# Optimization experiments

Hardware: AMD Instinct MI355X
Metric: run time of the kernel (lower is better)

## Reference

```python
import jax, jax.numpy as jnp
import numpy as np

B, C, L, T = 8, 512, 2048, 64

def setup_inputs() -> dict:
    key = jax.random.key(0)
    k1, k2, k3 = jax.random.split(key, 3)
    x = jax.random.normal(k1, (B, C, 1, L), dtype=jnp.float32)
    W1 = jax.random.normal(k2, (T, C), dtype=jnp.float32) * (1.0 / np.sqrt(C))
    W2 = jax.random.normal(k3, (T, C), dtype=jnp.float32) * (1.0 / np.sqrt(C))
    gamma = jnp.ones((1, 1), dtype=jnp.float32)
    ranges = 0  # unused by forward
    return {"x": x, "W1": W1, "W2": W2, "gamma": gamma, "ranges": ranges}

def reference(x, W1, W2, gamma, ranges):
    temp = x[:, :, 0, :]                                  # (B, C, L)
    q = jnp.einsum('tc,bcl->btl', W1, temp)               # conv1x1 -> (B, T, L)
    k = jnp.einsum('tc,bcl->btl', W2, temp)               # conv1x1 -> (B, T, L)
    scores = jnp.einsum('btl,btm->blm', q, k)             # Q^T K -> (B, L, L)
    attn = jax.nn.softmax(scores, axis=2)                 # softmax over last dim
    # temp @ attn^T: out[:, :, j] = sum_i attn[j, i] * temp[:, :, i]
    out = jnp.einsum('bci,bji->bcj', temp, attn)          # (B, C, L)
    out = temp + gamma[0, 0] * out                        # gamma scale + residual
    return out[:, :, None, :]                             # (B, C, 1, L)
```

## Files before the change

### kernel.cpp

```cpp
#include <hip/hip_runtime.h>
#include <cstddef>

#define BB 8
#define CC 512
#define LL 2048
#define TT 64

typedef short short8 __attribute__((ext_vector_type(8)));
typedef float floatx4 __attribute__((ext_vector_type(4)));
typedef unsigned short b16u;
typedef unsigned int u32;

static __device__ __forceinline__ unsigned f2bfu(float f) {
    unsigned u = __float_as_uint(f);
    u += 0x7fffu + ((u >> 16) & 1u);
    return u >> 16;
}
static __device__ __forceinline__ float bfu2f(unsigned h) {
    return __uint_as_float(h << 16);
}

#define MFMA16(a, b, c) __builtin_amdgcn_mfma_f32_16x16x32_bf16((a), (b), (c), 0, 0, 0)

__global__ __launch_bounds__(256) void wcvt_kernel(
    const float* __restrict__ W1, const float* __restrict__ W2,
    b16u* __restrict__ W1h, b16u* __restrict__ W1l,
    b16u* __restrict__ W2h, b16u* __restrict__ W2l)
{
    int flat = blockIdx.x * 256 + threadIdx.x;
    float4 v1 = *(const float4*)(W1 + (size_t)flat * 4);
    float4 v2 = *(const float4*)(W2 + (size_t)flat * 4);
    const float* e1 = (const float*)&v1;
    const float* e2 = (const float*)&v2;
    unsigned h1[4], l1[4], h2[4], l2[4];
#pragma unroll
    for (int k = 0; k < 4; ++k) {
        h1[k] = f2bfu(e1[k]); l1[k] = f2bfu(e1[k] - bfu2f(h1[k]));
        h2[k] = f2bfu(e2[k]); l2[k] = f2bfu(e2[k] - bfu2f(h2[k]));
    }
    uint2 a, b, c, d;
    a.x = h1[0] | (h1[1] << 16); a.y = h1[2] | (h1[3] << 16);
    b.x = l1[0] | (l1[1] << 16); b.y = l1[2] | (l1[3] << 16);
    c.x = h2[0] | (h2[1] << 16); c.y = h2[2] | (h2[3] << 16);
    d.x = l2[0] | (l2[1] << 16); d.y = l2[2] | (l2[3] << 16);
    *(uint2*)(W1h + (size_t)flat * 4) = a;
    *(uint2*)(W1l + (size_t)flat * 4) = b;
    *(uint2*)(W2h + (size_t)flat * 4) = c;
    *(uint2*)(W2l + (size_t)flat * 4) = d;
}

__global__ __launch_bounds__(256) void qkcvt_kernel(
    const float* __restrict__ x,
    const b16u* __restrict__ W1h, const b16u* __restrict__ W1l,
    const b16u* __restrict__ W2h, const b16u* __restrict__ W2l,
    b16u* __restrict__ Qt, b16u* __restrict__ Kt)
{
    __shared__ b16u Sxh[64 * 72];
    __shared__ b16u Sxl[64 * 72];
    __shared__ b16u S1h[64 * 72];
    __shared__ b16u S1l[64 * 72];
    __shared__ b16u S2h[64 * 72];
    __shared__ b16u S2l[64 * 72];
    const int b  = blockIdx.y;
    const int l0 = blockIdx.x * 64;
    const int tid = threadIdx.x;
    const int lane = tid & 63;
    const int w = tid >> 6;
    const int n16 = lane & 15;
    const int qd = lane >> 4;
    const float* xb = x + (size_t)b * CC * LL;

    const int cx = tid >> 2;
    const int sx = tid & 3;

    float4 xreg[4];
#pragma unroll
    for (int p = 0; p < 4; ++p)
        xreg[p] = *(const float4*)(xb + (size_t)cx * LL + l0 + (sx * 4 + p) * 4);

    floatx4 aq[4], ak[4];
#pragma unroll
    for (int nt = 0; nt < 4; ++nt) {
        aq[nt] = (floatx4){0.f, 0.f, 0.f, 0.f};
        ak[nt] = (floatx4){0.f, 0.f, 0.f, 0.f};
    }

    for (int c0 = 0; c0 < 512; c0 += 64) {
        __syncthreads();
#pragma unroll
        for (int p = 0; p < 4; ++p) {
            const float* e = (const float*)&xreg[p];
            int lbase = (sx * 4 + p) * 4;
#pragma unroll
            for (int k = 0; k < 4; ++k) {
                unsigned h = f2bfu(e[k]);
                unsigned lo = f2bfu(e[k] - bfu2f(h));
                Sxh[(lbase + k) * 72 + cx] = (b16u)h;
                Sxl[(lbase + k) * 72 + cx] = (b16u)lo;
            }
        }
#pragma unroll
        for (int p = 0; p < 2; ++p) {
            int flat = tid + p * 256;
            int t = flat >> 3, s8 = flat & 7;
            size_t off = (size_t)t * 512 + c0 + s8 * 8;
            *(uint4*)&S1h[t * 72 + s8 * 8] = *(const uint4*)(W1h + off);
            *(uint4*)&S1l[t * 72 + s8 * 8] = *(const uint4*)(W1l + off);
            *(uint4*)&S2h[t * 72 + s8 * 8] = *(const uint4*)(W2h + off);
            *(uint4*)&S2l[t * 72 + s8 * 8] = *(const uint4*)(W2l + off);
        }
        __syncthreads();
        if (c0 < 448) {
#pragma unroll
            for (int p = 0; p < 4; ++p)
                xreg[p] = *(const float4*)(xb + (size_t)(c0 + 64 + cx) * LL +
                                           l0 + (sx * 4 + p) * 4);
        }
#pragma unroll
        for (int kc = 0; kc < 2; ++kc) {
            const int ao = (w * 16 + n16) * 72 + kc * 32 + qd * 8;
            short8 a1h = *(const short8*)&S1h[ao];
            short8 a1l = *(const short8*)&S1l[ao];
            short8 a2h = *(const short8*)&S2h[ao];
            short8 a2l = *(const short8*)&S2l[ao];
#pragma unroll
            for (int nt = 0; nt < 4; ++nt) {
                const int bo = (nt * 16 + n16) * 72 + kc * 32 + qd * 8;
                short8 bh = *(const short8*)&Sxh[bo];
                short8 bl = *(const short8*)&Sxl[bo];
                aq[nt] = MFMA16(a1h, bh, aq[nt]);
                aq[nt] = MFMA16(a1h, bl, aq[nt]);
                aq[nt] = MFMA16(a1l, bh, aq[nt]);
                ak[nt] = MFMA16(a2h, bh, ak[nt]);
                ak[nt] = MFMA16(a2h, bl, ak[nt]);
                ak[nt] = MFMA16(a2l, bh, ak[nt]);
            }
        }
    }
#pragma unroll
    for (int nt = 0; nt < 4; ++nt) {
        int l = l0 + nt * 16 + n16;
        uint2 pq, pk;
        pq.x = f2bfu(aq[nt][0]) | (f2bfu(aq[nt][1]) << 16);
        pq.y = f2bfu(aq[nt][2]) | (f2bfu(aq[nt][3]) << 16);
        pk.x = f2bfu(ak[nt][0]) | (f2bfu(ak[nt][1]) << 16);
        pk.y = f2bfu(ak[nt][2]) | (f2bfu(ak[nt][3]) << 16);
        *(uint2*)(Qt + ((size_t)(b * 2048) + l) * 64 + w * 16 + qd * 4) = pq;
        *(uint2*)(Kt + ((size_t)(b * 2048) + l) * 64 + w * 16 + qd * 4) = pk;
    }
}

__global__ __launch_bounds__(256) void xcvt_kernel(
    const float* __restrict__ x, b16u* __restrict__ XT)
{
    int flat = blockIdx.x * 256 + threadIdx.x;
    int i4 = flat & 15;
    int t  = (flat >> 4) & 31;
    int c  = (flat >> 9) & 511;
    int b  = flat >> 18;
    float4 v = *(const float4*)(x + ((size_t)(b * 512 + c)) * 2048 + t * 64 + i4 * 4);
    uint2 wv;
    wv.x = f2bfu(v.x) | (f2bfu(v.y) << 16);
    wv.y = f2bfu(v.z) | (f2bfu(v.w) << 16);
    *(uint2*)(XT + (((size_t)(b * 32) + t) * 512 + c) * 64 + i4 * 4) = wv;
}

__global__ __launch_bounds__(512, 2) void fused_kernel(
    const float* __restrict__ x, const b16u* __restrict__ XT,
    const b16u* __restrict__ Qt, const b16u* __restrict__ Kt,
    const float* __restrict__ gamma, float* __restrict__ out)
{
    __shared__ __align__(16) char smem[139776];
    b16u*  Ps = (b16u*)smem;
    float* Zw = (float*)(smem + 32768);
    float* Zf = (float*)(smem + 139264);

    const int bid = blockIdx.x;
    const int b   = bid & 7;
    const int c0  = ((bid >> 3) & 1) * 256;
    const int j0  = (bid >> 4) * 128;
    const int tid = threadIdx.x;
    const int lane = tid & 63;
    const int w    = tid >> 6;
    const int n16  = lane & 15;
    const int qd   = lane >> 4;
    const int wi   = w & 3;
    const int wh   = w >> 2;

    const b16u* Qb = Qt + ((size_t)(b * LL) + j0 + wh * 64 + n16) * 64 + qd * 8;
    const b16u* Kb = Kt + ((size_t)(b * LL) + wi * 16 + n16) * 64 + qd * 8;
    const b16u* Vb = XT + (size_t)b * (32 * 512 * 64) +
                     ((size_t)(c0 + wi * 64 + n16)) * 64 + qd * 8;

    short8 qf[4][2];
#pragma unroll
    for (int nt2 = 0; nt2 < 4; ++nt2)
#pragma unroll
        for (int kc = 0; kc < 2; ++kc)
            qf[nt2][kc] = *(const short8*)(Qb + nt2 * (16 * 64) + kc * 32);

    floatx4 acc[4][4];
#pragma unroll
    for (int mt = 0; mt < 4; ++mt)
#pragma unroll
        for (int nt = 0; nt < 4; ++nt) acc[mt][nt] = (floatx4){0.f, 0.f, 0.f, 0.f};
    float zacc[4] = {0.f, 0.f, 0.f, 0.f};

#define KLOAD(KR, T)                                                       \
    {                                                                      \
        const b16u* kp = Kb + (size_t)(T) * (64 * 64);                     \
        KR[0] = *(const short8*)(kp);                                      \
        KR[1] = *(const short8*)(kp + 32);                                 \
    }

#define VLOAD(VR, T)                                                       \
    {                                                                      \
        const b16u* vp = Vb + (size_t)(T) * 32768;                         \
        _Pragma("unroll")                                                  \
        for (int mt = 0; mt < 4; ++mt) {                                   \
            VR[mt][0] = *(const short8*)(vp + mt * 1024);                  \
            VR[mt][1] = *(const short8*)(vp + mt * 1024 + 32);             \
        }                                                                  \
    }

#define SSTEP(PSOFF, KR)                                                   \
    {                                                                      \
        _Pragma("unroll")                                                  \
        for (int nt2 = 0; nt2 < 4; ++nt2) {                                \
            floatx4 sacc = (floatx4){0.f, 0.f, 0.f, 0.f};                  \
            sacc = MFMA16(KR[0], qf[nt2][0], sacc);                        \
            sacc = MFMA16(KR[1], qf[nt2][1], sacc);                        \
            float p0 = __expf(sacc[0] - 20.0f);                            \
            float p1 = __expf(sacc[1] - 20.0f);                            \
            float p2 = __expf(sacc[2] - 20.0f);                            \
            float p3 = __expf(sacc[3] - 20.0f);                            \
            zacc[nt2] += (p0 + p1) + (p2 + p3);                            \
            uint2 pk;                                                      \
            pk.x = f2bfu(p0) | (f2bfu(p1) << 16);                          \
            pk.y = f2bfu(p2) | (f2bfu(p3) << 16);                          \
            int jl = wh * 64 + nt2 * 16 + n16;                             \
            int phys = (wi * 2 + (qd >> 1)) ^ (n16 & 7);                   \
            *(uint2*)&Ps[(PSOFF) + jl * 64 + phys * 8 + (qd & 1) * 4] = pk;\
        }                                                                  \
    }

#define PVSTEP(PSOFF, VR)                                                  \
    {                                                                      \
        __builtin_amdgcn_s_setprio(1);                                     \
        _Pragma("unroll")                                                  \
        for (int kc = 0; kc < 2; ++kc) {                                   \
            short8 bfr[4];                                                 \
            _Pragma("unroll")                                              \
            for (int nt = 0; nt < 4; ++nt) {                               \
                int phys = (kc * 4 + qd) ^ (n16 & 7);                      \
                bfr[nt] = *(const short8*)&Ps[(PSOFF) +                    \
                    (wh * 64 + nt * 16 + n16) * 64 + phys * 8];            \
            }                                                              \
            _Pragma("unroll")                                              \
            for (int mt = 0; mt < 4; ++mt)                                 \
                _Pragma("unroll")                                          \
                for (int nt = 0; nt < 4; ++nt)                             \
                    acc[mt][nt] = MFMA16(VR[mt][kc], bfr[nt], acc[mt][nt]);\
        }                                                                  \
        __builtin_amdgcn_s_setprio(0);                                     \
    }

    short8 kA[2], kB[2], kT[2];
    short8 v0[4][2], v1[4][2];

    KLOAD(kT, 0)
    VLOAD(v0, 0)
    SSTEP(0, kT)
    KLOAD(kA, 1)
    __syncthreads();

    for (int tt = 0; tt < 32; tt += 2) {
        VLOAD(v1, tt + 1)
        if (tt + 2 < 32) KLOAD(kB, tt + 2)
        SSTEP(8192, kA)
        PVSTEP(0, v0)
        __syncthreads();
        if (tt + 2 < 32) {
            VLOAD(v0, tt + 2)
            if (tt + 3 < 32) KLOAD(kA, tt + 3)
            SSTEP(0, kB)
        }
        PVSTEP(8192, v1)
        __syncthreads();
    }
#undef KLOAD
#undef VLOAD
#undef SSTEP
#undef PVSTEP

#pragma unroll
    for (int nt2 = 0; nt2 < 4; ++nt2) {
        float z = zacc[nt2];
        z += __shfl_xor(z, 16);
        z += __shfl_xor(z, 32);
        if (qd == 0) Zw[w * 64 + nt2 * 16 + n16] = z;
    }
    __syncthreads();
    if (tid < 128) {
        int hb = (tid >> 6) * 4;
        Zf[tid] = Zw[(hb + 0) * 64 + (tid & 63)] + Zw[(hb + 1) * 64 + (tid & 63)] +
                  Zw[(hb + 2) * 64 + (tid & 63)] + Zw[(hb + 3) * 64 + (tid & 63)];
    }
    __syncthreads();

    const float g = gamma[0];
    float* st = (float*)(smem + w * 17408);
#pragma unroll
    for (int nt = 0; nt < 4; ++nt) {
        float zi = g / Zf[wh * 64 + nt * 16 + n16];
#pragma unroll
        for (int mt = 0; mt < 4; ++mt)
#pragma unroll
            for (int r = 0; r < 4; ++r)
                st[(mt * 16 + qd * 4 + r) * 68 + nt * 16 + n16] = acc[mt][nt][r] * zi;
    }
    __syncthreads();
#pragma unroll
    for (int p = 0; p < 16; ++p) {
        int rl = qd * 16 + p;
        int cg = c0 + wi * 64 + rl;
        size_t go = ((size_t)(b * CC) + cg) * 2048 + j0 + wh * 64 + n16 * 4;
        float4 v = *(const float4*)&st[rl * 68 + n16 * 4];
        float4 xv = *(const float4*)(x + go);
        v.x += xv.x; v.y += xv.y; v.z += xv.z; v.w += xv.w;
        *(float4*)(out + go) = v;
    }
}

extern "C" void kernel_launch(void* const* d_in, const int* in_sizes, int n_in,
                              void* d_out, int out_size, void* d_ws, size_t ws_size,
                              hipStream_t stream)
{
    (void)in_sizes; (void)n_in; (void)out_size; (void)ws_size;
    const float* x     = (const float*)d_in[0];
    const float* W1    = (const float*)d_in[1];
    const float* W2    = (const float*)d_in[2];
    const float* gamma = (const float*)d_in[3];
    float* out = (float*)d_out;

    b16u* Qt  = (b16u*)d_ws;
    b16u* Kt  = Qt  + (size_t)BB * LL * TT;
    b16u* W1h = Kt  + (size_t)BB * LL * TT;
    b16u* W1l = W1h + (size_t)TT * CC;
    b16u* W2h = W1l + (size_t)TT * CC;
    b16u* W2l = W2h + (size_t)TT * CC;
    b16u* XT  = W2l + (size_t)TT * CC;

    wcvt_kernel <<<dim3(32),      256, 0, stream>>>(W1, W2, W1h, W1l, W2h, W2l);
    xcvt_kernel <<<dim3(8192),    256, 0, stream>>>(x, XT);
    qkcvt_kernel<<<dim3(32, BB),  256, 0, stream>>>(x, W1h, W1l, W2h, W2l, Qt, Kt);
    fused_kernel<<<dim3(256),     512, 0, stream>>>(x, XT, Qt, Kt, gamma, out);
}
```

Baseline: 193.2 us.

## Warp-specialize fused attention into score producers and PV consumers

The fused kernel now runs 12 waves per block. Four producer waves compute QK scores, exponentiate them and write bf16 P tiles into a double-buffered LDS region. Eight consumer waves load V and run the PV MFMAs over all 512 channels for a 64-column query tile. This removes the duplicated score and exp work that the old per-channel-half blocks repeated. The trade-off is that each block now streams twice as much V per query column, and producers and consumers must stay balanced across the barriers.

```diff
diff --git a/kernel.cpp b/kernel.cpp
--- a/kernel.cpp
+++ b/kernel.cpp
@@ -165,86 +165,75 @@
     *(uint2*)(XT + (((size_t)(b * 32) + t) * 512 + c) * 64 + i4 * 4) = wv;
 }
 
-__global__ __launch_bounds__(512, 2) void fused_kernel(
+__global__ __launch_bounds__(768, 3) void fused_kernel(
     const float* __restrict__ x, const b16u* __restrict__ XT,
     const b16u* __restrict__ Qt, const b16u* __restrict__ Kt,
     const float* __restrict__ gamma, float* __restrict__ out)
 {
-    __shared__ __align__(16) char smem[139776];
+    __shared__ __align__(16) char smem[140544];
     b16u*  Ps = (b16u*)smem;
-    float* Zw = (float*)(smem + 32768);
-    float* Zf = (float*)(smem + 139264);
+    float* Zw = (float*)(smem + 139264);
+    float* Zf = (float*)(smem + 140288);
 
     const int bid = blockIdx.x;
     const int b   = bid & 7;
-    const int c0  = ((bid >> 3) & 1) * 256;
-    const int j0  = (bid >> 4) * 128;
+    const int j0  = (bid >> 3) * 64;
     const int tid = threadIdx.x;
     const int lane = tid & 63;
     const int w    = tid >> 6;
     const int n16  = lane & 15;
     const int qd   = lane >> 4;
-    const int wi   = w & 3;
-    const int wh   = w >> 2;
-
-    const b16u* Qb = Qt + ((size_t)(b * LL) + j0 + wh * 64 + n16) * 64 + qd * 8;
-    const b16u* Kb = Kt + ((size_t)(b * LL) + wi * 16 + n16) * 64 + qd * 8;
-    const b16u* Vb = XT + (size_t)b * (32 * 512 * 64) +
-                     ((size_t)(c0 + wi * 64 + n16)) * 64 + qd * 8;
+
+    const b16u* Qb = Qt + ((size_t)(b * LL) + j0 + n16) * 64 + qd * 8;
+    const b16u* Kb = Kt + ((size_t)(b * LL) + (w & 3) * 16 + n16) * 64 + qd * 8;
+    const b16u* Vb = XT + (size_t)b * (32 * 32768) +
+                     ((size_t)((w - 4) * 64 + n16)) * 64 + qd * 8;
 
     short8 qf[4][2];
-#pragma unroll
-    for (int nt2 = 0; nt2 < 4; ++nt2)
-#pragma unroll
-        for (int kc = 0; kc < 2; ++kc)
-            qf[nt2][kc] = *(const short8*)(Qb + nt2 * (16 * 64) + kc * 32);
-
+    short8 kA[2], kB[2];
+    float  zacc[4] = {0.f, 0.f, 0.f, 0.f};
     floatx4 acc[4][4];
-#pragma unroll
-    for (int mt = 0; mt < 4; ++mt)
-#pragma unroll
-        for (int nt = 0; nt < 4; ++nt) acc[mt][nt] = (floatx4){0.f, 0.f, 0.f, 0.f};
-    float zacc[4] = {0.f, 0.f, 0.f, 0.f};
+    short8 av[4][2];
 
 #define KLOAD(KR, T)                                                       \
     {                                                                      \
-        const b16u* kp = Kb + (size_t)(T) * (64 * 64);                     \
+        const b16u* kp = Kb + (size_t)(T) * 4096;                          \
         KR[0] = *(const short8*)(kp);                                      \
         KR[1] = *(const short8*)(kp + 32);                                 \
     }
 
-#define VLOAD(VR, T)                                                       \
+#define VLOAD(T)                                                           \
     {                                                                      \
         const b16u* vp = Vb + (size_t)(T) * 32768;                         \
         _Pragma("unroll")                                                  \
         for (int mt = 0; mt < 4; ++mt) {                                   \
-            VR[mt][0] = *(const short8*)(vp + mt * 1024);                  \
-            VR[mt][1] = *(const short8*)(vp + mt * 1024 + 32);             \
+            av[mt][0] = *(const short8*)(vp + mt * 1024);                  \
+            av[mt][1] = *(const short8*)(vp + mt * 1024 + 32);             \
         }                                                                  \
     }
 
 #define SSTEP(PSOFF, KR)                                                   \
     {                                                                      \
         _Pragma("unroll")                                                  \
-        for (int nt2 = 0; nt2 < 4; ++nt2) {                                \
+        for (int nt = 0; nt < 4; ++nt) {                                   \
             floatx4 sacc = (floatx4){0.f, 0.f, 0.f, 0.f};                  \
-            sacc = MFMA16(KR[0], qf[nt2][0], sacc);                        \
-            sacc = MFMA16(KR[1], qf[nt2][1], sacc);                        \
+            sacc = MFMA16(KR[0], qf[nt][0], sacc);                         \
+            sacc = MFMA16(KR[1], qf[nt][1], sacc);                         \
             float p0 = __expf(sacc[0] - 20.0f);                            \
             float p1 = __expf(sacc[1] - 20.0f);                            \
             float p2 = __expf(sacc[2] - 20.0f);                            \
             float p3 = __expf(sacc[3] - 20.0f);                            \
-            zacc[nt2] += (p0 + p1) + (p2 + p3);                            \
+            zacc[nt] += (p0 + p1) + (p2 + p3);                             \
             uint2 pk;                                                      \
             pk.x = f2bfu(p0) | (f2bfu(p1) << 16);                          \
             pk.y = f2bfu(p2) | (f2bfu(p3) << 16);                          \
-            int jl = wh * 64 + nt2 * 16 + n16;                             \
-            int phys = (wi * 2 + (qd >> 1)) ^ (n16 & 7);                   \
+            int jl = nt * 16 + n16;                                        \
+            int phys = ((w & 3) * 2 + (qd >> 1)) ^ (n16 & 7);              \
             *(uint2*)&Ps[(PSOFF) + jl * 64 + phys * 8 + (qd & 1) * 4] = pk;\
         }                                                                  \
     }
 
-#define PVSTEP(PSOFF, VR)                                                  \
+#define PVSTEP(PSOFF)                                                      \
     {                                                                      \
         __builtin_amdgcn_s_setprio(1);                                     \
         _Pragma("unroll")                                                  \
@@ -254,38 +243,54 @@
             for (int nt = 0; nt < 4; ++nt) {                               \
                 int phys = (kc * 4 + qd) ^ (n16 & 7);                      \
                 bfr[nt] = *(const short8*)&Ps[(PSOFF) +                    \
-                    (wh * 64 + nt * 16 + n16) * 64 + phys * 8];            \
+                    (nt * 16 + n16) * 64 + phys * 8];                      \
             }                                                              \
             _Pragma("unroll")                                              \
             for (int mt = 0; mt < 4; ++mt)                                 \
                 _Pragma("unroll")                                          \
                 for (int nt = 0; nt < 4; ++nt)                             \
-                    acc[mt][nt] = MFMA16(VR[mt][kc], bfr[nt], acc[mt][nt]);\
+                    acc[mt][nt] = MFMA16(av[mt][kc], bfr[nt], acc[mt][nt]);\
         }                                                                  \
         __builtin_amdgcn_s_setprio(0);                                     \
     }
 
-    short8 kA[2], kB[2], kT[2];
-    short8 v0[4][2], v1[4][2];
-
-    KLOAD(kT, 0)
-    VLOAD(v0, 0)
-    SSTEP(0, kT)
-    KLOAD(kA, 1)
+    if (w < 4) {
+#pragma unroll
+        for (int nt = 0; nt < 4; ++nt) {
+            qf[nt][0] = *(const short8*)(Qb + nt * 1024);
+            qf[nt][1] = *(const short8*)(Qb + nt * 1024 + 32);
+        }
+        KLOAD(kA, 0)
+        SSTEP(0, kA)
+        KLOAD(kA, 1)
+    } else {
+#pragma unroll
+        for (int mt = 0; mt < 4; ++mt)
+#pragma unroll
+            for (int nt = 0; nt < 4; ++nt)
+                acc[mt][nt] = (floatx4){0.f, 0.f, 0.f, 0.f};
+        VLOAD(0)
+    }
     __syncthreads();
 
     for (int tt = 0; tt < 32; tt += 2) {
-        VLOAD(v1, tt + 1)
-        if (tt + 2 < 32) KLOAD(kB, tt + 2)
-        SSTEP(8192, kA)
-        PVSTEP(0, v0)
+        if (w < 4) {
+            SSTEP(4096, kA)
+            if (tt + 2 < 32) KLOAD(kB, tt + 2)
+        } else {
+            PVSTEP(0)
+            VLOAD(tt + 1)
+        }
         __syncthreads();
-        if (tt + 2 < 32) {
-            VLOAD(v0, tt + 2)
-            if (tt + 3 < 32) KLOAD(kA, tt + 3)
-            SSTEP(0, kB)
-        }
-        PVSTEP(8192, v1)
+        if (w < 4) {
+            if (tt + 2 < 32) {
+                SSTEP(0, kB)
+                if (tt + 3 < 32) KLOAD(kA, tt + 3)
+            }
+        } else {
+            PVSTEP(4096)
+            if (tt + 2 < 32) VLOAD(tt + 2)
+        }
         __syncthreads();
     }
 #undef KLOAD
@@ -293,42 +298,47 @@
 #undef SSTEP
 #undef PVSTEP
 
-#pragma unroll
-    for (int nt2 = 0; nt2 < 4; ++nt2) {
-        float z = zacc[nt2];
-        z += __shfl_xor(z, 16);
-        z += __shfl_xor(z, 32);
-        if (qd == 0) Zw[w * 64 + nt2 * 16 + n16] = z;
+    if (w < 4) {
+#pragma unroll
+        for (int nt = 0; nt < 4; ++nt) {
+            float z = zacc[nt];
+            z += __shfl_xor(z, 16);
+            z += __shfl_xor(z, 32);
+            if (qd == 0) Zw[w * 64 + nt * 16 + n16] = z;
+        }
     }
     __syncthreads();
-    if (tid < 128) {
-        int hb = (tid >> 6) * 4;
-        Zf[tid] = Zw[(hb + 0) * 64 + (tid & 63)] + Zw[(hb + 1) * 64 + (tid & 63)] +
-                  Zw[(hb + 2) * 64 + (tid & 63)] + Zw[(hb + 3) * 64 + (tid & 63)];
-    }
+    if (tid < 64)
+        Zf[tid] = Zw[tid] + Zw[64 + tid] + Zw[128 + tid] + Zw[192 + tid];
     __syncthreads();
 
     const float g = gamma[0];
-    float* st = (float*)(smem + w * 17408);
-#pragma unroll
-    for (int nt = 0; nt < 4; ++nt) {
-        float zi = g / Zf[wh * 64 + nt * 16 + n16];
-#pragma unroll
-        for (int mt = 0; mt < 4; ++mt)
-#pragma unroll
-            for (int r = 0; r < 4; ++r)
-                st[(mt * 16 + qd * 4 + r) * 68 + nt * 16 + n16] = acc[mt][nt][r] * zi;
+    if (w >= 4) {
+        float* st = (float*)(smem + (w - 4) * 17408);
+#pragma unroll
+        for (int nt = 0; nt < 4; ++nt) {
+            float zi = g / Zf[nt * 16 + n16];
+#pragma unroll
+            for (int mt = 0; mt < 4; ++mt)
+#pragma unroll
+                for (int r = 0; r < 4; ++r)
+                    st[(mt * 16 + qd * 4 + r) * 68 + nt * 16 + n16] =
+                        acc[mt][nt][r] * zi;
+        }
     }
     __syncthreads();
-#pragma unroll
-    for (int p = 0; p < 16; ++p) {
-        int rl = qd * 16 + p;
-        int cg = c0 + wi * 64 + rl;
-        size_t go = ((size_t)(b * CC) + cg) * 2048 + j0 + wh * 64 + n16 * 4;
-        float4 v = *(const float4*)&st[rl * 68 + n16 * 4];
-        float4 xv = *(const float4*)(x + go);
-        v.x += xv.x; v.y += xv.y; v.z += xv.z; v.w += xv.w;
-        *(float4*)(out + go) = v;
+    if (w >= 4) {
+        const float* st = (const float*)(smem + (w - 4) * 17408);
+#pragma unroll
+        for (int p = 0; p < 16; ++p) {
+            int rl = qd * 16 + p;
+            int cg = (w - 4) * 64 + rl;
+            size_t go = ((size_t)(b * CC) + cg) * 2048 + j0 + n16 * 4;
+            float4 v = *(const float4*)&st[rl * 68 + n16 * 4];
+            float4 xv = *(const float4*)(x + go);
+            v.x += xv.x; v.y += xv.y; v.z += xv.z; v.w += xv.w;
+            *(float4*)(out + go) = v;
+        }
     }
 }
 
@@ -354,5 +364,5 @@
     wcvt_kernel <<<dim3(32),      256, 0, stream>>>(W1, W2, W1h, W1l, W2h, W2l);
     xcvt_kernel <<<dim3(8192),    256, 0, stream>>>(x, XT);
     qkcvt_kernel<<<dim3(32, BB),  256, 0, stream>>>(x, W1h, W1l, W2h, W2l, Qt, Kt);
-    fused_kernel<<<dim3(256),     512, 0, stream>>>(x, XT, Qt, Kt, gamma, out);
-}
+    fused_kernel<<<dim3(256),     768, 0, stream>>>(x, XT, Qt, Kt, gamma, out);
+}
```

Measured after the change: 205.5 us. +6.4%, slower.
